# Kernel optimization log

Measured on AMD Instinct MI355X. Metric: run time of the kernel, lower is better.

## Reference

```python
import jax, jax.numpy as jnp
import numpy as np

NEG_SLOPE = 0.2
EPS = 1e-16


def gat_conv(x, src, dst, W, a_src, a_dst, b, num_nodes):
    # Single-head PyG GATConv (heads=1, add_self_loops already applied via src/dst).
    h = x @ W                                   # [N, C]
    alpha_s = h @ a_src                         # [N]
    alpha_d = h @ a_dst                         # [N]
    e = jax.nn.leaky_relu(alpha_s[src] + alpha_d[dst], NEG_SLOPE)  # [E]
    # softmax over incoming edges per destination node
    m = jax.ops.segment_max(e, dst, num_segments=num_nodes)        # [N]
    ex = jnp.exp(e - m[dst])
    denom = jax.ops.segment_sum(ex, dst, num_segments=num_nodes)   # [N]
    alpha = ex / (denom[dst] + EPS)                                 # [E]
    out = jax.ops.segment_sum(h[src] * alpha[:, None], dst, num_segments=num_nodes)
    return out + b


def setup_inputs() -> dict:
    key = jax.random.key(0)
    ks = jax.random.split(key, 10)
    N, E, F_in, H, C = 100000, 1600000, 64, 64, 32
    x = jax.random.normal(ks[0], (N, F_in), dtype=jnp.float32)
    edge_index = jax.random.randint(ks[1], (2, E), 0, N, dtype=jnp.int64)
    s1 = 1.0 / np.sqrt(F_in)
    s2 = 1.0 / np.sqrt(H)
    return {
        "x": x,
        "edge_index": edge_index,
        "W1": jax.random.normal(ks[2], (F_in, H), dtype=jnp.float32) * s1,
        "a1_src": jax.random.normal(ks[3], (H,), dtype=jnp.float32) * s2,
        "a1_dst": jax.random.normal(ks[4], (H,), dtype=jnp.float32) * s2,
        "b1": jnp.zeros((H,), dtype=jnp.float32),
        "W2": jax.random.normal(ks[5], (H, C), dtype=jnp.float32) * s2,
        "a2_src": jax.random.normal(ks[6], (C,), dtype=jnp.float32) / np.sqrt(C),
        "a2_dst": jax.random.normal(ks[7], (C,), dtype=jnp.float32) / np.sqrt(C),
        "b2": jnp.zeros((C,), dtype=jnp.float32),
    }


def reference(x, edge_index, W1, a1_src, a1_dst, b1, W2, a2_src, a2_dst, b2):
    N = x.shape[0]
    loops = jnp.arange(N, dtype=edge_index.dtype)
    src = jnp.concatenate([edge_index[0], loops])  # add self-loops (GATConv default)
    dst = jnp.concatenate([edge_index[1], loops])
    # dropout layers are no-ops in eval mode
    h = jax.nn.relu(gat_conv(x, src, dst, W1, a1_src, a1_dst, b1, N))
    out = gat_conv(h, src, dst, W2, a2_src, a2_dst, b2, N)
    return jax.nn.log_softmax(out, axis=-1)
```

## Files before the change

kernel.cpp:

```cpp
#include <hip/hip_runtime.h>

typedef unsigned int uint;
typedef unsigned short ushort;
typedef short short8 __attribute__((ext_vector_type(8)));
typedef float floatx4 __attribute__((ext_vector_type(4)));

#define LEAKY(e) ((e) > 0.f ? (e) : 0.2f * (e))
#define BCAP 6144
#define EPT 32
#define TILE (256 * EPT)

__device__ __forceinline__ ushort f2bf(float f) {
    uint u = __float_as_uint(f);
    return (ushort)((u + 0x7fffu + ((u >> 16) & 1u)) >> 16);
}
__device__ __forceinline__ uint pack2bf(float lo, float hi) {
    return (uint)f2bf(lo) | ((uint)f2bf(hi) << 16);
}
__device__ __forceinline__ float bflo(uint u) { return __uint_as_float(u << 16); }
__device__ __forceinline__ float bfhi(uint u) { return __uint_as_float(u & 0xffff0000u); }

__device__ __forceinline__ void binK_body(
    int bid, const int* __restrict__ srcA, const int* __restrict__ dstA,
    int* __restrict__ bcur, int* __restrict__ binned, int E, int Etot, int nbuck)
{
    __shared__ int hist[512];
    __shared__ int basep[512];
    int t = threadIdx.x;
    long long start = (long long)bid * TILE;

    hist[t] = 0; hist[t + 256] = 0;
    __syncthreads();

    short bs[EPT];
    int vals[EPT];
#pragma unroll
    for (int j = 0; j < EPT; ++j) {
        long long i = start + (long long)j * 256 + t;
        if (i < Etot) {
            int s, d;
            if (i < E) { s = srcA[i]; d = dstA[i]; } else { s = d = (int)(i - E); }
            int b = d >> 8;
            bs[j] = (short)b;
            vals[j] = (s << 8) | (d & 255);
            atomicAdd(&hist[b], 1);
        } else bs[j] = -1;
    }
    __syncthreads();

    for (int b = t; b < nbuck; b += 256) {
        int hc = hist[b];
        basep[b] = hc ? atomicAdd(bcur + b * 16, hc) : 0;
    }
    __syncthreads();
    hist[t] = 0; hist[t + 256] = 0;
    __syncthreads();

#pragma unroll
    for (int j = 0; j < EPT; ++j) {
        int b = bs[j];
        if (b >= 0) {
            int pos = basep[b] + atomicAdd(&hist[b], 1);
            if (pos < BCAP) binned[(size_t)b * BCAP + pos] = vals[j];
        }
    }
}

__device__ __forceinline__ void gemm1_body(
    int bid, const float* __restrict__ x, const float* __restrict__ W,
    const float* __restrict__ a_src, const float* __restrict__ a_dst,
    ushort* __restrict__ hb, float* __restrict__ as, float* __restrict__ ad, int N)
{
    int tid = threadIdx.x;
    int wave = tid >> 6, lane = tid & 63;
    int q = lane >> 4, c0 = lane & 15;
    int rowbase = bid * 64 + wave * 16;
    int arow = rowbase + c0;
    bool aok = arow < N;

    short8 afrag[2];
#pragma unroll
    for (int kb = 0; kb < 2; ++kb) {
        float xa[8];
        if (aok) {
            const float4 u0 = *(const float4*)(x + (size_t)arow * 64 + kb * 32 + q * 8);
            const float4 u1 = *(const float4*)(x + (size_t)arow * 64 + kb * 32 + q * 8 + 4);
            xa[0] = u0.x; xa[1] = u0.y; xa[2] = u0.z; xa[3] = u0.w;
            xa[4] = u1.x; xa[5] = u1.y; xa[6] = u1.z; xa[7] = u1.w;
        } else {
#pragma unroll
            for (int j = 0; j < 8; ++j) xa[j] = 0.f;
        }
#pragma unroll
        for (int j = 0; j < 8; ++j) afrag[kb][j] = (short)f2bf(xa[j]);
    }

    short8 bfrag[4][2];
#pragma unroll
    for (int t = 0; t < 4; ++t)
#pragma unroll
        for (int kb = 0; kb < 2; ++kb)
#pragma unroll
            for (int j = 0; j < 8; ++j)
                bfrag[t][kb][j] = (short)f2bf(W[(size_t)(kb * 32 + q * 8 + j) * 64 + t * 16 + c0]);

    floatx4 acc[4];
#pragma unroll
    for (int t = 0; t < 4; ++t) acc[t] = (floatx4){0.f, 0.f, 0.f, 0.f};
#pragma unroll
    for (int t = 0; t < 4; ++t)
#pragma unroll
        for (int kb = 0; kb < 2; ++kb)
            acc[t] = __builtin_amdgcn_mfma_f32_16x16x32_bf16(afrag[kb], bfrag[t][kb], acc[t], 0, 0, 0);

    float a_s[4], a_d[4];
#pragma unroll
    for (int t = 0; t < 4; ++t) { a_s[t] = a_src[t * 16 + c0]; a_d[t] = a_dst[t * 16 + c0]; }
    float vs[4], vd[4];
#pragma unroll
    for (int r = 0; r < 4; ++r) {
        vs[r] = 0.f; vd[r] = 0.f;
#pragma unroll
        for (int t = 0; t < 4; ++t) { vs[r] += acc[t][r] * a_s[t]; vd[r] += acc[t][r] * a_d[t]; }
    }
#pragma unroll
    for (int o = 1; o < 16; o <<= 1)
#pragma unroll
        for (int r = 0; r < 4; ++r) {
            vs[r] += __shfl_xor(vs[r], o, 16);
            vd[r] += __shfl_xor(vd[r], o, 16);
        }
    int drow = rowbase + q * 4;
    if (c0 == 0) {
#pragma unroll
        for (int r = 0; r < 4; ++r)
            if (drow + r < N) { as[drow + r] = vs[r]; ad[drow + r] = vd[r]; }
    }
#pragma unroll
    for (int r = 0; r < 4; ++r) {
        if (drow + r < N) {
#pragma unroll
            for (int t = 0; t < 4; ++t)
                hb[(size_t)(drow + r) * 64 + t * 16 + c0] = f2bf(acc[t][r]);
        }
    }
}

__global__ __launch_bounds__(256) void fusedK(
    const int* __restrict__ srcA, const int* __restrict__ dstA,
    int* __restrict__ bcur, int* __restrict__ binned, int E, int Etot, int nbuck, int tb,
    const float* __restrict__ x, const float* __restrict__ W,
    const float* __restrict__ a_src, const float* __restrict__ a_dst,
    ushort* __restrict__ hb, float* __restrict__ as, float* __restrict__ ad, int N)
{
    int b = (int)blockIdx.x;
    if (b < tb) binK_body(b, srcA, dstA, bcur, binned, E, Etot, nbuck);
    else gemm1_body(b - tb, x, W, a_src, a_dst, hb, as, ad, N);
}

__global__ __launch_bounds__(256) void gemm2_mfma(
    const ushort* __restrict__ aggb, const float* __restrict__ b1,
    const float* __restrict__ W,
    const float* __restrict__ a_src, const float* __restrict__ a_dst,
    ushort* __restrict__ hb, float* __restrict__ as, float* __restrict__ ad, int N)
{
    int tid = threadIdx.x;
    int wave = tid >> 6, lane = tid & 63;
    int q = lane >> 4, c0 = lane & 15;
    int rowbase = blockIdx.x * 64 + wave * 16;
    int arow = rowbase + c0;
    bool aok = arow < N;

    short8 afrag[2];
#pragma unroll
    for (int kb = 0; kb < 2; ++kb) {
        float xa[8];
        const float4 b0 = *(const float4*)(b1 + kb * 32 + q * 8);
        const float4 b4 = *(const float4*)(b1 + kb * 32 + q * 8 + 4);
        if (aok) {
            const uint4 u = *(const uint4*)(aggb + (size_t)arow * 64 + kb * 32 + q * 8);
            xa[0] = bflo(u.x) + b0.x; xa[1] = bfhi(u.x) + b0.y;
            xa[2] = bflo(u.y) + b0.z; xa[3] = bfhi(u.y) + b0.w;
            xa[4] = bflo(u.z) + b4.x; xa[5] = bfhi(u.z) + b4.y;
            xa[6] = bflo(u.w) + b4.z; xa[7] = bfhi(u.w) + b4.w;
#pragma unroll
            for (int j = 0; j < 8; ++j) xa[j] = xa[j] > 0.f ? xa[j] : 0.f;
        } else {
#pragma unroll
            for (int j = 0; j < 8; ++j) xa[j] = 0.f;
        }
#pragma unroll
        for (int j = 0; j < 8; ++j) afrag[kb][j] = (short)f2bf(xa[j]);
    }

    short8 bfrag[2][2];
#pragma unroll
    for (int t = 0; t < 2; ++t)
#pragma unroll
        for (int kb = 0; kb < 2; ++kb)
#pragma unroll
            for (int j = 0; j < 8; ++j)
                bfrag[t][kb][j] = (short)f2bf(W[(size_t)(kb * 32 + q * 8 + j) * 32 + t * 16 + c0]);

    floatx4 acc[2];
#pragma unroll
    for (int t = 0; t < 2; ++t) acc[t] = (floatx4){0.f, 0.f, 0.f, 0.f};
#pragma unroll
    for (int t = 0; t < 2; ++t)
#pragma unroll
        for (int kb = 0; kb < 2; ++kb)
            acc[t] = __builtin_amdgcn_mfma_f32_16x16x32_bf16(afrag[kb], bfrag[t][kb], acc[t], 0, 0, 0);

    float a_s[2], a_d[2];
#pragma unroll
    for (int t = 0; t < 2; ++t) { a_s[t] = a_src[t * 16 + c0]; a_d[t] = a_dst[t * 16 + c0]; }
    float vs[4], vd[4];
#pragma unroll
    for (int r = 0; r < 4; ++r) {
        vs[r] = 0.f; vd[r] = 0.f;
#pragma unroll
        for (int t = 0; t < 2; ++t) { vs[r] += acc[t][r] * a_s[t]; vd[r] += acc[t][r] * a_d[t]; }
    }
#pragma unroll
    for (int o = 1; o < 16; o <<= 1)
#pragma unroll
        for (int r = 0; r < 4; ++r) {
            vs[r] += __shfl_xor(vs[r], o, 16);
            vd[r] += __shfl_xor(vd[r], o, 16);
        }
    int drow = rowbase + q * 4;
    if (c0 == 0) {
#pragma unroll
        for (int r = 0; r < 4; ++r)
            if (drow + r < N) { as[drow + r] = vs[r]; ad[drow + r] = vd[r]; }
    }
#pragma unroll
    for (int r = 0; r < 4; ++r) {
        if (drow + r < N) {
#pragma unroll
            for (int t = 0; t < 2; ++t)
                hb[(size_t)(drow + r) * 32 + t * 16 + c0] = f2bf(acc[t][r]);
        }
    }
}

__global__ __launch_bounds__(256) void bucketK(
    const int* __restrict__ bcur, const int* __restrict__ binned,
    int* __restrict__ off, int* __restrict__ csr, int N, int nbuck)
{
    __shared__ int hist[256];
    __shared__ int sh[256];
    __shared__ int cur[256];
    int b = blockIdx.x;
    int t = threadIdx.x;
    int cnt = min(bcur[b * 16], BCAP);
    const int* bin = binned + (size_t)b * BCAP;

    int partial = 0;
    for (int i = t; i < b; i += 256) partial += min(bcur[i * 16], BCAP);
    sh[t] = partial;
    __syncthreads();
#pragma unroll
    for (int o = 128; o > 0; o >>= 1) {
        if (t < o) sh[t] += sh[t + o];
        __syncthreads();
    }
    int base = sh[0];
    __syncthreads();

    hist[t] = 0;
    __syncthreads();
    for (int i = t; i < cnt; i += 256) atomicAdd(&hist[bin[i] & 255], 1);
    __syncthreads();
    int v = hist[t];
    sh[t] = v;
    __syncthreads();
#pragma unroll
    for (int o = 1; o < 256; o <<= 1) {
        int u = (t >= o) ? sh[t - o] : 0;
        __syncthreads();
        sh[t] += u;
        __syncthreads();
    }
    int excl = sh[t] - v;
    int d = b * 256 + t;
    if (d < N) off[d] = base + excl;
    if (b == nbuck - 1 && t == 0) off[N] = base + cnt;
    cur[t] = base + excl;
    __syncthreads();
    for (int i = t; i < cnt; i += 256) {
        int e = bin[i];
        int p = atomicAdd(&cur[e & 255], 1);
        csr[p] = e >> 8;
    }
}

__global__ __launch_bounds__(256) void node_agg1(
    const int* __restrict__ csr_src, const int* __restrict__ off,
    const float* __restrict__ as, const float* __restrict__ ad,
    const ushort* __restrict__ hb, ushort* __restrict__ aggb, int N)
{
    int tid = threadIdx.x;
    int lid = tid & 7;
    int n = blockIdx.x * 32 + (tid >> 3);
    if (n >= N) return;
    int p0 = off[n], p1 = off[n + 1];
    float adn = ad[n];

    float den = 0.f;
    float acc[8];
#pragma unroll
    for (int k = 0; k < 8; ++k) acc[k] = 0.f;

    int base = p0;
    for (; base + 8 <= p1; base += 8) {
        int s_l = csr_src[base + lid];
        float a_l = as[s_l];
        uint4 v[8];
#pragma unroll
        for (int j = 0; j < 8; ++j) {
            int s_j = __shfl(s_l, j, 8);
            v[j] = *(const uint4*)(hb + (size_t)s_j * 64 + lid * 8);
        }
        float w_l = __expf(LEAKY(a_l + adn));
        den += w_l;
#pragma unroll
        for (int j = 0; j < 8; ++j) {
            float w = __shfl(w_l, j, 8);
            acc[0] += w * bflo(v[j].x); acc[1] += w * bfhi(v[j].x);
            acc[2] += w * bflo(v[j].y); acc[3] += w * bfhi(v[j].y);
            acc[4] += w * bflo(v[j].z); acc[5] += w * bfhi(v[j].z);
            acc[6] += w * bflo(v[j].w); acc[7] += w * bfhi(v[j].w);
        }
    }
    int r = p1 - base;
    if (r) {
        int s_l = 0; float w_l = 0.f;
        if (lid < r) { s_l = csr_src[base + lid]; w_l = __expf(LEAKY(as[s_l] + adn)); }
        den += w_l;
#pragma unroll
        for (int j = 0; j < 8; ++j) {
            if (j < r) {
                int s_j = __shfl(s_l, j, 8);
                float w = __shfl(w_l, j, 8);
                const uint4 v = *(const uint4*)(hb + (size_t)s_j * 64 + lid * 8);
                acc[0] += w * bflo(v.x); acc[1] += w * bfhi(v.x);
                acc[2] += w * bflo(v.y); acc[3] += w * bfhi(v.y);
                acc[4] += w * bflo(v.z); acc[5] += w * bfhi(v.z);
                acc[6] += w * bflo(v.w); acc[7] += w * bfhi(v.w);
            }
        }
    }
#pragma unroll
    for (int o = 4; o > 0; o >>= 1) den += __shfl_xor(den, o, 8);
    float inv = 1.f / den;
    uint4 o4;
    o4.x = pack2bf(acc[0] * inv, acc[1] * inv);
    o4.y = pack2bf(acc[2] * inv, acc[3] * inv);
    o4.z = pack2bf(acc[4] * inv, acc[5] * inv);
    o4.w = pack2bf(acc[6] * inv, acc[7] * inv);
    *(uint4*)(aggb + (size_t)n * 64 + lid * 8) = o4;
}

__global__ __launch_bounds__(256) void node_agg2(
    const int* __restrict__ csr_src, const int* __restrict__ off,
    const float* __restrict__ as, const float* __restrict__ ad,
    const ushort* __restrict__ hb, const float* __restrict__ b2,
    float* __restrict__ out, int N)
{
    int tid = threadIdx.x;
    int lid = tid & 3;
    int n = blockIdx.x * 64 + (tid >> 2);
    if (n >= N) return;
    int p0 = off[n], p1 = off[n + 1];
    float adn = ad[n];

    float den = 0.f;
    float acc[8];
#pragma unroll
    for (int k = 0; k < 8; ++k) acc[k] = 0.f;

    int base = p0;
    for (; base + 4 <= p1; base += 4) {
        int s_l = csr_src[base + lid];
        float a_l = as[s_l];
        uint4 v[4];
#pragma unroll
        for (int j = 0; j < 4; ++j) {
            int s_j = __shfl(s_l, j, 4);
            v[j] = *(const uint4*)(hb + (size_t)s_j * 32 + lid * 8);
        }
        float w_l = __expf(LEAKY(a_l + adn));
        den += w_l;
#pragma unroll
        for (int j = 0; j < 4; ++j) {
            float w = __shfl(w_l, j, 4);
            acc[0] += w * bflo(v[j].x); acc[1] += w * bfhi(v[j].x);
            acc[2] += w * bflo(v[j].y); acc[3] += w * bfhi(v[j].y);
            acc[4] += w * bflo(v[j].z); acc[5] += w * bfhi(v[j].z);
            acc[6] += w * bflo(v[j].w); acc[7] += w * bfhi(v[j].w);
        }
    }
    int r = p1 - base;
    if (r) {
        int s_l = 0; float w_l = 0.f;
        if (lid < r) { s_l = csr_src[base + lid]; w_l = __expf(LEAKY(as[s_l] + adn)); }
        den += w_l;
#pragma unroll
        for (int j = 0; j < 4; ++j) {
            if (j < r) {
                int s_j = __shfl(s_l, j, 4);
                float w = __shfl(w_l, j, 4);
                const uint4 v = *(const uint4*)(hb + (size_t)s_j * 32 + lid * 8);
                acc[0] += w * bflo(v.x); acc[1] += w * bfhi(v.x);
                acc[2] += w * bflo(v.y); acc[3] += w * bfhi(v.y);
                acc[4] += w * bflo(v.z); acc[5] += w * bfhi(v.z);
                acc[6] += w * bflo(v.w); acc[7] += w * bfhi(v.w);
            }
        }
    }
#pragma unroll
    for (int o = 2; o > 0; o >>= 1) den += __shfl_xor(den, o, 4);
    float inv = 1.f / den;
#pragma unroll
    for (int k = 0; k < 8; ++k) acc[k] = acc[k] * inv + b2[lid * 8 + k];

    float mx = acc[0];
#pragma unroll
    for (int k = 1; k < 8; ++k) mx = fmaxf(mx, acc[k]);
#pragma unroll
    for (int o = 2; o > 0; o >>= 1) mx = fmaxf(mx, __shfl_xor(mx, o, 4));
    float se = 0.f;
#pragma unroll
    for (int k = 0; k < 8; ++k) se += __expf(acc[k] - mx);
#pragma unroll
    for (int o = 2; o > 0; o >>= 1) se += __shfl_xor(se, o, 4);
    float lse = mx + __logf(se);
    float4 o0 = make_float4(acc[0] - lse, acc[1] - lse, acc[2] - lse, acc[3] - lse);
    float4 o1 = make_float4(acc[4] - lse, acc[5] - lse, acc[6] - lse, acc[7] - lse);
    float* op = out + (size_t)n * 32 + lid * 8;
    *(float4*)op = o0;
    *(float4*)(op + 4) = o1;
}

extern "C" void kernel_launch(void* const* d_in, const int* in_sizes, int n_in,
                              void* d_out, int out_size, void* d_ws, size_t ws_size,
                              hipStream_t stream) {
    const float* x   = (const float*)d_in[0];
    const int*   ei  = (const int*)d_in[1];
    const float* W1  = (const float*)d_in[2];
    const float* a1s = (const float*)d_in[3];
    const float* a1d = (const float*)d_in[4];
    const float* b1  = (const float*)d_in[5];
    const float* W2  = (const float*)d_in[6];
    const float* a2s = (const float*)d_in[7];
    const float* a2d = (const float*)d_in[8];
    const float* b2  = (const float*)d_in[9];

    int N = in_sizes[0] / 64;
    int E = in_sizes[1] / 2;
    int Etot = E + N;
    int nbuck = (N + 255) >> 8;
    const int* srcA = ei;
    const int* dstA = ei + E;

    float* ws = (float*)d_ws;
    ushort* hb1  = (ushort*)ws;
    ushort* aggb = hb1 + (size_t)N * 64;
    ushort* hb2  = aggb + (size_t)N * 64;
    float* as1   = ws + (size_t)N * (32 + 32 + 16);
    float* ad1   = as1 + N;
    float* as2   = ad1 + N;
    float* ad2   = as2 + N;
    int* off     = (int*)(ad2 + N);
    int* bcur    = off + (N + 1);
    int* csr     = bcur + (size_t)nbuck * 16;
    int* binned  = csr + Etot;

    hipMemsetAsync(bcur, 0, sizeof(int) * (size_t)nbuck * 16, stream);

    int tb = (int)(((long long)Etot + TILE - 1) / TILE);
    int g1 = (N + 63) / 64;

    fusedK<<<tb + g1, 256, 0, stream>>>(srcA, dstA, bcur, binned, E, Etot, nbuck, tb,
                                        x, W1, a1s, a1d, hb1, as1, ad1, N);
    bucketK<<<nbuck, 256, 0, stream>>>(bcur, binned, off, csr, N, nbuck);
    node_agg1<<<(N + 31) / 32, 256, 0, stream>>>(csr, off, as1, ad1, hb1, aggb, N);
    gemm2_mfma<<<g1, 256, 0, stream>>>(aggb, b1, W2, a2s, a2d, hb2, as2, ad2, N);
    node_agg2<<<(N + 63) / 64, 256, 0, stream>>>(csr, off, as2, ad2, hb2, b2,
                                                 (float*)d_out, N);
}
```

Baseline: 213.2 us.

## Fuse layer-1 aggregation with layer-2 GEMM into a single MFMA kernel

Merges node_agg1 and gemm2_mfma into one kernel. Each wave aggregates 16 destination nodes, with lanes laid out to match the MFMA A-fragment, so the aggregated features stay in registers and feed the layer-2 bf16 MFMA directly. This removes the write and re-read of the bf16 intermediate aggregation buffer and one kernel launch. The cost is a different gather pattern: 4 edges per iteration per node, a ballot-driven loop that runs to the highest degree among the wave's 16 nodes (divergence), and more registers per thread.

```diff
diff --git a/kernel.cpp b/kernel.cpp
--- a/kernel.cpp
+++ b/kernel.cpp
@@ -13,9 +13,6 @@
 __device__ __forceinline__ ushort f2bf(float f) {
     uint u = __float_as_uint(f);
     return (ushort)((u + 0x7fffu + ((u >> 16) & 1u)) >> 16);
-}
-__device__ __forceinline__ uint pack2bf(float lo, float hi) {
-    return (uint)f2bf(lo) | ((uint)f2bf(hi) << 16);
 }
 __device__ __forceinline__ float bflo(uint u) { return __uint_as_float(u << 16); }
 __device__ __forceinline__ float bfhi(uint u) { return __uint_as_float(u & 0xffff0000u); }
@@ -158,92 +155,6 @@
     else gemm1_body(b - tb, x, W, a_src, a_dst, hb, as, ad, N);
 }
 
-__global__ __launch_bounds__(256) void gemm2_mfma(
-    const ushort* __restrict__ aggb, const float* __restrict__ b1,
-    const float* __restrict__ W,
-    const float* __restrict__ a_src, const float* __restrict__ a_dst,
-    ushort* __restrict__ hb, float* __restrict__ as, float* __restrict__ ad, int N)
-{
-    int tid = threadIdx.x;
-    int wave = tid >> 6, lane = tid & 63;
-    int q = lane >> 4, c0 = lane & 15;
-    int rowbase = blockIdx.x * 64 + wave * 16;
-    int arow = rowbase + c0;
-    bool aok = arow < N;
-
-    short8 afrag[2];
-#pragma unroll
-    for (int kb = 0; kb < 2; ++kb) {
-        float xa[8];
-        const float4 b0 = *(const float4*)(b1 + kb * 32 + q * 8);
-        const float4 b4 = *(const float4*)(b1 + kb * 32 + q * 8 + 4);
-        if (aok) {
-            const uint4 u = *(const uint4*)(aggb + (size_t)arow * 64 + kb * 32 + q * 8);
-            xa[0] = bflo(u.x) + b0.x; xa[1] = bfhi(u.x) + b0.y;
-            xa[2] = bflo(u.y) + b0.z; xa[3] = bfhi(u.y) + b0.w;
-            xa[4] = bflo(u.z) + b4.x; xa[5] = bfhi(u.z) + b4.y;
-            xa[6] = bflo(u.w) + b4.z; xa[7] = bfhi(u.w) + b4.w;
-#pragma unroll
-            for (int j = 0; j < 8; ++j) xa[j] = xa[j] > 0.f ? xa[j] : 0.f;
-        } else {
-#pragma unroll
-            for (int j = 0; j < 8; ++j) xa[j] = 0.f;
-        }
-#pragma unroll
-        for (int j = 0; j < 8; ++j) afrag[kb][j] = (short)f2bf(xa[j]);
-    }
-
-    short8 bfrag[2][2];
-#pragma unroll
-    for (int t = 0; t < 2; ++t)
-#pragma unroll
-        for (int kb = 0; kb < 2; ++kb)
-#pragma unroll
-            for (int j = 0; j < 8; ++j)
-                bfrag[t][kb][j] = (short)f2bf(W[(size_t)(kb * 32 + q * 8 + j) * 32 + t * 16 + c0]);
-
-    floatx4 acc[2];
-#pragma unroll
-    for (int t = 0; t < 2; ++t) acc[t] = (floatx4){0.f, 0.f, 0.f, 0.f};
-#pragma unroll
-    for (int t = 0; t < 2; ++t)
-#pragma unroll
-        for (int kb = 0; kb < 2; ++kb)
-            acc[t] = __builtin_amdgcn_mfma_f32_16x16x32_bf16(afrag[kb], bfrag[t][kb], acc[t], 0, 0, 0);
-
-    float a_s[2], a_d[2];
-#pragma unroll
-    for (int t = 0; t < 2; ++t) { a_s[t] = a_src[t * 16 + c0]; a_d[t] = a_dst[t * 16 + c0]; }
-    float vs[4], vd[4];
-#pragma unroll
-    for (int r = 0; r < 4; ++r) {
-        vs[r] = 0.f; vd[r] = 0.f;
-#pragma unroll
-        for (int t = 0; t < 2; ++t) { vs[r] += acc[t][r] * a_s[t]; vd[r] += acc[t][r] * a_d[t]; }
-    }
-#pragma unroll
-    for (int o = 1; o < 16; o <<= 1)
-#pragma unroll
-        for (int r = 0; r < 4; ++r) {
-            vs[r] += __shfl_xor(vs[r], o, 16);
-            vd[r] += __shfl_xor(vd[r], o, 16);
-        }
-    int drow = rowbase + q * 4;
-    if (c0 == 0) {
-#pragma unroll
-        for (int r = 0; r < 4; ++r)
-            if (drow + r < N) { as[drow + r] = vs[r]; ad[drow + r] = vd[r]; }
-    }
-#pragma unroll
-    for (int r = 0; r < 4; ++r) {
-        if (drow + r < N) {
-#pragma unroll
-            for (int t = 0; t < 2; ++t)
-                hb[(size_t)(drow + r) * 32 + t * 16 + c0] = f2bf(acc[t][r]);
-        }
-    }
-}
-
 __global__ __launch_bounds__(256) void bucketK(
     const int* __restrict__ bcur, const int* __restrict__ binned,
     int* __restrict__ off, int* __restrict__ csr, int N, int nbuck)
@@ -295,71 +206,119 @@
     }
 }
 
-__global__ __launch_bounds__(256) void node_agg1(
-    const int* __restrict__ csr_src, const int* __restrict__ off,
+__global__ __launch_bounds__(256) void agg1gemm2K(
+    const int* __restrict__ csr, const int* __restrict__ off,
     const float* __restrict__ as, const float* __restrict__ ad,
-    const ushort* __restrict__ hb, ushort* __restrict__ aggb, int N)
+    const ushort* __restrict__ hb1, const float* __restrict__ b1,
+    const float* __restrict__ W,
+    const float* __restrict__ a_src, const float* __restrict__ a_dst,
+    ushort* __restrict__ hb2, float* __restrict__ as2, float* __restrict__ ad2, int N)
 {
     int tid = threadIdx.x;
-    int lid = tid & 7;
-    int n = blockIdx.x * 32 + (tid >> 3);
-    if (n >= N) return;
-    int p0 = off[n], p1 = off[n + 1];
-    float adn = ad[n];
+    int wave = tid >> 6, lane = tid & 63;
+    int q = lane >> 4, m = lane & 15;
+    int rowbase = blockIdx.x * 64 + wave * 16;
+    int n = rowbase + m;
+    int nc = (n < N) ? n : N - 1;
+    int p0 = off[nc];
+    int deg = (n < N) ? (off[nc + 1] - p0) : 0;
+    float adn = (n < N) ? ad[n] : 0.f;
 
     float den = 0.f;
-    float acc[8];
-#pragma unroll
-    for (int k = 0; k < 8; ++k) acc[k] = 0.f;
-
-    int base = p0;
-    for (; base + 8 <= p1; base += 8) {
-        int s_l = csr_src[base + lid];
-        float a_l = as[s_l];
-        uint4 v[8];
-#pragma unroll
-        for (int j = 0; j < 8; ++j) {
-            int s_j = __shfl(s_l, j, 8);
-            v[j] = *(const uint4*)(hb + (size_t)s_j * 64 + lid * 8);
-        }
-        float w_l = __expf(LEAKY(a_l + adn));
+    float acc0[8], acc1[8];
+#pragma unroll
+    for (int k = 0; k < 8; ++k) { acc0[k] = 0.f; acc1[k] = 0.f; }
+
+    int base = 0;
+    while (__ballot(base < deg)) {
+        bool valid = (base + q) < deg;
+        int s_l = valid ? csr[p0 + base + q] : 0;
+        float w_l = valid ? __expf(LEAKY(as[s_l] + adn)) : 0.f;
         den += w_l;
-#pragma unroll
-        for (int j = 0; j < 8; ++j) {
-            float w = __shfl(w_l, j, 8);
-            acc[0] += w * bflo(v[j].x); acc[1] += w * bfhi(v[j].x);
-            acc[2] += w * bflo(v[j].y); acc[3] += w * bfhi(v[j].y);
-            acc[4] += w * bflo(v[j].z); acc[5] += w * bfhi(v[j].z);
-            acc[6] += w * bflo(v[j].w); acc[7] += w * bfhi(v[j].w);
-        }
-    }
-    int r = p1 - base;
-    if (r) {
-        int s_l = 0; float w_l = 0.f;
-        if (lid < r) { s_l = csr_src[base + lid]; w_l = __expf(LEAKY(as[s_l] + adn)); }
-        den += w_l;
-#pragma unroll
-        for (int j = 0; j < 8; ++j) {
-            if (j < r) {
-                int s_j = __shfl(s_l, j, 8);
-                float w = __shfl(w_l, j, 8);
-                const uint4 v = *(const uint4*)(hb + (size_t)s_j * 64 + lid * 8);
-                acc[0] += w * bflo(v.x); acc[1] += w * bfhi(v.x);
-                acc[2] += w * bflo(v.y); acc[3] += w * bfhi(v.y);
-                acc[4] += w * bflo(v.z); acc[5] += w * bfhi(v.z);
-                acc[6] += w * bflo(v.w); acc[7] += w * bfhi(v.w);
-            }
-        }
-    }
-#pragma unroll
-    for (int o = 4; o > 0; o >>= 1) den += __shfl_xor(den, o, 8);
+        int sj[4];
+        uint4 va[4], vb[4];
+#pragma unroll
+        for (int j = 0; j < 4; ++j) {
+            sj[j] = __shfl(s_l, m | (j << 4), 64);
+            va[j] = *(const uint4*)(hb1 + (size_t)sj[j] * 64 + q * 8);
+            vb[j] = *(const uint4*)(hb1 + (size_t)sj[j] * 64 + 32 + q * 8);
+        }
+#pragma unroll
+        for (int j = 0; j < 4; ++j) {
+            float w = __shfl(w_l, m | (j << 4), 64);
+            acc0[0] += w * bflo(va[j].x); acc0[1] += w * bfhi(va[j].x);
+            acc0[2] += w * bflo(va[j].y); acc0[3] += w * bfhi(va[j].y);
+            acc0[4] += w * bflo(va[j].z); acc0[5] += w * bfhi(va[j].z);
+            acc0[6] += w * bflo(va[j].w); acc0[7] += w * bfhi(va[j].w);
+            acc1[0] += w * bflo(vb[j].x); acc1[1] += w * bfhi(vb[j].x);
+            acc1[2] += w * bflo(vb[j].y); acc1[3] += w * bfhi(vb[j].y);
+            acc1[4] += w * bflo(vb[j].z); acc1[5] += w * bfhi(vb[j].z);
+            acc1[6] += w * bflo(vb[j].w); acc1[7] += w * bfhi(vb[j].w);
+        }
+        base += 4;
+    }
+    den += __shfl_xor(den, 16, 64);
+    den += __shfl_xor(den, 32, 64);
     float inv = 1.f / den;
-    uint4 o4;
-    o4.x = pack2bf(acc[0] * inv, acc[1] * inv);
-    o4.y = pack2bf(acc[2] * inv, acc[3] * inv);
-    o4.z = pack2bf(acc[4] * inv, acc[5] * inv);
-    o4.w = pack2bf(acc[6] * inv, acc[7] * inv);
-    *(uint4*)(aggb + (size_t)n * 64 + lid * 8) = o4;
+
+    short8 afrag[2];
+#pragma unroll
+    for (int j = 0; j < 8; ++j) {
+        float x0 = acc0[j] * inv + b1[q * 8 + j];
+        float x1 = acc1[j] * inv + b1[32 + q * 8 + j];
+        afrag[0][j] = (short)f2bf(x0 > 0.f ? x0 : 0.f);
+        afrag[1][j] = (short)f2bf(x1 > 0.f ? x1 : 0.f);
+    }
+
+    short8 bfrag[2][2];
+#pragma unroll
+    for (int t = 0; t < 2; ++t)
+#pragma unroll
+        for (int kb = 0; kb < 2; ++kb)
+#pragma unroll
+            for (int j = 0; j < 8; ++j)
+                bfrag[t][kb][j] = (short)f2bf(W[(size_t)(kb * 32 + q * 8 + j) * 32 + t * 16 + m]);
+
+    floatx4 acc[2];
+#pragma unroll
+    for (int t = 0; t < 2; ++t) acc[t] = (floatx4){0.f, 0.f, 0.f, 0.f};
+#pragma unroll
+    for (int t = 0; t < 2; ++t)
+#pragma unroll
+        for (int kb = 0; kb < 2; ++kb)
+            acc[t] = __builtin_amdgcn_mfma_f32_16x16x32_bf16(afrag[kb], bfrag[t][kb], acc[t], 0, 0, 0);
+
+    float a_s[2], a_d[2];
+#pragma unroll
+    for (int t = 0; t < 2; ++t) { a_s[t] = a_src[t * 16 + m]; a_d[t] = a_dst[t * 16 + m]; }
+    float vs[4], vd[4];
+#pragma unroll
+    for (int r = 0; r < 4; ++r) {
+        vs[r] = 0.f; vd[r] = 0.f;
+#pragma unroll
+        for (int t = 0; t < 2; ++t) { vs[r] += acc[t][r] * a_s[t]; vd[r] += acc[t][r] * a_d[t]; }
+    }
+#pragma unroll
+    for (int o = 1; o < 16; o <<= 1)
+#pragma unroll
+        for (int r = 0; r < 4; ++r) {
+            vs[r] += __shfl_xor(vs[r], o, 16);
+            vd[r] += __shfl_xor(vd[r], o, 16);
+        }
+    int drow = rowbase + q * 4;
+    if (m == 0) {
+#pragma unroll
+        for (int r = 0; r < 4; ++r)
+            if (drow + r < N) { as2[drow + r] = vs[r]; ad2[drow + r] = vd[r]; }
+    }
+#pragma unroll
+    for (int r = 0; r < 4; ++r) {
+        if (drow + r < N) {
+#pragma unroll
+            for (int t = 0; t < 2; ++t)
+                hb2[(size_t)(drow + r) * 32 + t * 16 + m] = f2bf(acc[t][r]);
+        }
+    }
 }
 
 __global__ __launch_bounds__(256) void node_agg2(
@@ -465,17 +424,16 @@
     const int* dstA = ei + E;
 
     float* ws = (float*)d_ws;
-    ushort* hb1  = (ushort*)ws;
-    ushort* aggb = hb1 + (size_t)N * 64;
-    ushort* hb2  = aggb + (size_t)N * 64;
-    float* as1   = ws + (size_t)N * (32 + 32 + 16);
-    float* ad1   = as1 + N;
-    float* as2   = ad1 + N;
-    float* ad2   = as2 + N;
-    int* off     = (int*)(ad2 + N);
-    int* bcur    = off + (N + 1);
-    int* csr     = bcur + (size_t)nbuck * 16;
-    int* binned  = csr + Etot;
+    ushort* hb1 = (ushort*)ws;
+    ushort* hb2 = hb1 + (size_t)N * 64;
+    float* as1  = ws + (size_t)N * 48;
+    float* ad1  = as1 + N;
+    float* as2  = ad1 + N;
+    float* ad2  = as2 + N;
+    int* off    = (int*)(ad2 + N);
+    int* bcur   = off + (N + 1);
+    int* csr    = bcur + (size_t)nbuck * 16;
+    int* binned = csr + Etot;
 
     hipMemsetAsync(bcur, 0, sizeof(int) * (size_t)nbuck * 16, stream);
 
@@ -485,8 +443,8 @@
     fusedK<<<tb + g1, 256, 0, stream>>>(srcA, dstA, bcur, binned, E, Etot, nbuck, tb,
                                         x, W1, a1s, a1d, hb1, as1, ad1, N);
     bucketK<<<nbuck, 256, 0, stream>>>(bcur, binned, off, csr, N, nbuck);
-    node_agg1<<<(N + 31) / 32, 256, 0, stream>>>(csr, off, as1, ad1, hb1, aggb, N);
-    gemm2_mfma<<<g1, 256, 0, stream>>>(aggb, b1, W2, a2s, a2d, hb2, as2, ad2, N);
+    agg1gemm2K<<<g1, 256, 0, stream>>>(csr, off, as1, ad1, hb1, b1, W2, a2s, a2d,
+                                       hb2, as2, ad2, N);
     node_agg2<<<(N + 63) / 64, 256, 0, stream>>>(csr, off, as2, ad2, hb2, b2,
                                                  (float*)d_out, N);
 }
```

Result: slower. 219.0 us (+2.7%).

## Fuse layer-1 aggregation with layer-2 MFMA GEMM via shared memory

Applied to the files above, without the earlier changes.

Merges node_agg1 and gemm2_mfma into one kernel. The per-node aggregated layer-1 features are staged in LDS in fp32 and then consumed by two waves running the 64x32 MFMA projection, bias, ReLU and attention-logit reductions. This removes one launch and the bf16 round trip of the N x 64 intermediate through global memory. In exchange, two of the four waves sit idle during the GEMM phase and the block needs a barrier and about 8.7 KB of LDS.

```diff
diff --git a/kernel.cpp b/kernel.cpp
--- a/kernel.cpp
+++ b/kernel.cpp
@@ -13,9 +13,6 @@
 __device__ __forceinline__ ushort f2bf(float f) {
     uint u = __float_as_uint(f);
     return (ushort)((u + 0x7fffu + ((u >> 16) & 1u)) >> 16);
-}
-__device__ __forceinline__ uint pack2bf(float lo, float hi) {
-    return (uint)f2bf(lo) | ((uint)f2bf(hi) << 16);
 }
 __device__ __forceinline__ float bflo(uint u) { return __uint_as_float(u << 16); }
 __device__ __forceinline__ float bfhi(uint u) { return __uint_as_float(u & 0xffff0000u); }
@@ -158,92 +155,6 @@
     else gemm1_body(b - tb, x, W, a_src, a_dst, hb, as, ad, N);
 }
 
-__global__ __launch_bounds__(256) void gemm2_mfma(
-    const ushort* __restrict__ aggb, const float* __restrict__ b1,
-    const float* __restrict__ W,
-    const float* __restrict__ a_src, const float* __restrict__ a_dst,
-    ushort* __restrict__ hb, float* __restrict__ as, float* __restrict__ ad, int N)
-{
-    int tid = threadIdx.x;
-    int wave = tid >> 6, lane = tid & 63;
-    int q = lane >> 4, c0 = lane & 15;
-    int rowbase = blockIdx.x * 64 + wave * 16;
-    int arow = rowbase + c0;
-    bool aok = arow < N;
-
-    short8 afrag[2];
-#pragma unroll
-    for (int kb = 0; kb < 2; ++kb) {
-        float xa[8];
-        const float4 b0 = *(const float4*)(b1 + kb * 32 + q * 8);
-        const float4 b4 = *(const float4*)(b1 + kb * 32 + q * 8 + 4);
-        if (aok) {
-            const uint4 u = *(const uint4*)(aggb + (size_t)arow * 64 + kb * 32 + q * 8);
-            xa[0] = bflo(u.x) + b0.x; xa[1] = bfhi(u.x) + b0.y;
-            xa[2] = bflo(u.y) + b0.z; xa[3] = bfhi(u.y) + b0.w;
-            xa[4] = bflo(u.z) + b4.x; xa[5] = bfhi(u.z) + b4.y;
-            xa[6] = bflo(u.w) + b4.z; xa[7] = bfhi(u.w) + b4.w;
-#pragma unroll
-            for (int j = 0; j < 8; ++j) xa[j] = xa[j] > 0.f ? xa[j] : 0.f;
-        } else {
-#pragma unroll
-            for (int j = 0; j < 8; ++j) xa[j] = 0.f;
-        }
-#pragma unroll
-        for (int j = 0; j < 8; ++j) afrag[kb][j] = (short)f2bf(xa[j]);
-    }
-
-    short8 bfrag[2][2];
-#pragma unroll
-    for (int t = 0; t < 2; ++t)
-#pragma unroll
-        for (int kb = 0; kb < 2; ++kb)
-#pragma unroll
-            for (int j = 0; j < 8; ++j)
-                bfrag[t][kb][j] = (short)f2bf(W[(size_t)(kb * 32 + q * 8 + j) * 32 + t * 16 + c0]);
-
-    floatx4 acc[2];
-#pragma unroll
-    for (int t = 0; t < 2; ++t) acc[t] = (floatx4){0.f, 0.f, 0.f, 0.f};
-#pragma unroll
-    for (int t = 0; t < 2; ++t)
-#pragma unroll
-        for (int kb = 0; kb < 2; ++kb)
-            acc[t] = __builtin_amdgcn_mfma_f32_16x16x32_bf16(afrag[kb], bfrag[t][kb], acc[t], 0, 0, 0);
-
-    float a_s[2], a_d[2];
-#pragma unroll
-    for (int t = 0; t < 2; ++t) { a_s[t] = a_src[t * 16 + c0]; a_d[t] = a_dst[t * 16 + c0]; }
-    float vs[4], vd[4];
-#pragma unroll
-    for (int r = 0; r < 4; ++r) {
-        vs[r] = 0.f; vd[r] = 0.f;
-#pragma unroll
-        for (int t = 0; t < 2; ++t) { vs[r] += acc[t][r] * a_s[t]; vd[r] += acc[t][r] * a_d[t]; }
-    }
-#pragma unroll
-    for (int o = 1; o < 16; o <<= 1)
-#pragma unroll
-        for (int r = 0; r < 4; ++r) {
-            vs[r] += __shfl_xor(vs[r], o, 16);
-            vd[r] += __shfl_xor(vd[r], o, 16);
-        }
-    int drow = rowbase + q * 4;
-    if (c0 == 0) {
-#pragma unroll
-        for (int r = 0; r < 4; ++r)
-            if (drow + r < N) { as[drow + r] = vs[r]; ad[drow + r] = vd[r]; }
-    }
-#pragma unroll
-    for (int r = 0; r < 4; ++r) {
-        if (drow + r < N) {
-#pragma unroll
-            for (int t = 0; t < 2; ++t)
-                hb[(size_t)(drow + r) * 32 + t * 16 + c0] = f2bf(acc[t][r]);
-        }
-    }
-}
-
 __global__ __launch_bounds__(256) void bucketK(
     const int* __restrict__ bcur, const int* __restrict__ binned,
     int* __restrict__ off, int* __restrict__ csr, int N, int nbuck)
@@ -295,71 +206,142 @@
     }
 }
 
-__global__ __launch_bounds__(256) void node_agg1(
+__global__ __launch_bounds__(256) void agg1gemm2K(
     const int* __restrict__ csr_src, const int* __restrict__ off,
     const float* __restrict__ as, const float* __restrict__ ad,
-    const ushort* __restrict__ hb, ushort* __restrict__ aggb, int N)
-{
+    const ushort* __restrict__ hb1, const float* __restrict__ b1,
+    const float* __restrict__ W,
+    const float* __restrict__ a_src, const float* __restrict__ a_dst,
+    ushort* __restrict__ hb2, float* __restrict__ as2, float* __restrict__ ad2, int N)
+{
+    __shared__ float aggL[32 * 68];
     int tid = threadIdx.x;
     int lid = tid & 7;
-    int n = blockIdx.x * 32 + (tid >> 3);
-    if (n >= N) return;
-    int p0 = off[n], p1 = off[n + 1];
-    float adn = ad[n];
+    int nl = tid >> 3;
+    int n = blockIdx.x * 32 + nl;
 
     float den = 0.f;
     float acc[8];
 #pragma unroll
     for (int k = 0; k < 8; ++k) acc[k] = 0.f;
 
-    int base = p0;
-    for (; base + 8 <= p1; base += 8) {
-        int s_l = csr_src[base + lid];
-        float a_l = as[s_l];
-        uint4 v[8];
+    if (n < N) {
+        int p0 = off[n], p1 = off[n + 1];
+        float adn = ad[n];
+        int base = p0;
+        for (; base + 8 <= p1; base += 8) {
+            int s_l = csr_src[base + lid];
+            float a_l = as[s_l];
+            uint4 v[8];
+#pragma unroll
+            for (int j = 0; j < 8; ++j) {
+                int s_j = __shfl(s_l, j, 8);
+                v[j] = *(const uint4*)(hb1 + (size_t)s_j * 64 + lid * 8);
+            }
+            float w_l = __expf(LEAKY(a_l + adn));
+            den += w_l;
+#pragma unroll
+            for (int j = 0; j < 8; ++j) {
+                float w = __shfl(w_l, j, 8);
+                acc[0] += w * bflo(v[j].x); acc[1] += w * bfhi(v[j].x);
+                acc[2] += w * bflo(v[j].y); acc[3] += w * bfhi(v[j].y);
+                acc[4] += w * bflo(v[j].z); acc[5] += w * bfhi(v[j].z);
+                acc[6] += w * bflo(v[j].w); acc[7] += w * bfhi(v[j].w);
+            }
+        }
+        int r = p1 - base;
+        if (r) {
+            int s_l = 0; float w_l = 0.f;
+            if (lid < r) { s_l = csr_src[base + lid]; w_l = __expf(LEAKY(as[s_l] + adn)); }
+            den += w_l;
+#pragma unroll
+            for (int j = 0; j < 8; ++j) {
+                if (j < r) {
+                    int s_j = __shfl(s_l, j, 8);
+                    float w = __shfl(w_l, j, 8);
+                    const uint4 v = *(const uint4*)(hb1 + (size_t)s_j * 64 + lid * 8);
+                    acc[0] += w * bflo(v.x); acc[1] += w * bfhi(v.x);
+                    acc[2] += w * bflo(v.y); acc[3] += w * bfhi(v.y);
+                    acc[4] += w * bflo(v.z); acc[5] += w * bfhi(v.z);
+                    acc[6] += w * bflo(v.w); acc[7] += w * bfhi(v.w);
+                }
+            }
+        }
+#pragma unroll
+        for (int o = 4; o > 0; o >>= 1) den += __shfl_xor(den, o, 8);
+    } else den = 1.f;
+
+    float inv = 1.f / den;
+    float4 o0 = make_float4(acc[0] * inv, acc[1] * inv, acc[2] * inv, acc[3] * inv);
+    float4 o1 = make_float4(acc[4] * inv, acc[5] * inv, acc[6] * inv, acc[7] * inv);
+    *(float4*)&aggL[nl * 68 + lid * 8] = o0;
+    *(float4*)&aggL[nl * 68 + lid * 8 + 4] = o1;
+    __syncthreads();
+
+    int wave = tid >> 6, lane = tid & 63;
+    if (wave >= 2) return;
+    int q = lane >> 4, m = lane & 15;
+    int rowbase = blockIdx.x * 32 + wave * 16;
+
+    short8 afrag[2];
+#pragma unroll
+    for (int kb = 0; kb < 2; ++kb) {
 #pragma unroll
         for (int j = 0; j < 8; ++j) {
-            int s_j = __shfl(s_l, j, 8);
-            v[j] = *(const uint4*)(hb + (size_t)s_j * 64 + lid * 8);
-        }
-        float w_l = __expf(LEAKY(a_l + adn));
-        den += w_l;
-#pragma unroll
-        for (int j = 0; j < 8; ++j) {
-            float w = __shfl(w_l, j, 8);
-            acc[0] += w * bflo(v[j].x); acc[1] += w * bfhi(v[j].x);
-            acc[2] += w * bflo(v[j].y); acc[3] += w * bfhi(v[j].y);
-            acc[4] += w * bflo(v[j].z); acc[5] += w * bfhi(v[j].z);
-            acc[6] += w * bflo(v[j].w); acc[7] += w * bfhi(v[j].w);
-        }
-    }
-    int r = p1 - base;
-    if (r) {
-        int s_l = 0; float w_l = 0.f;
-        if (lid < r) { s_l = csr_src[base + lid]; w_l = __expf(LEAKY(as[s_l] + adn)); }
-        den += w_l;
-#pragma unroll
-        for (int j = 0; j < 8; ++j) {
-            if (j < r) {
-                int s_j = __shfl(s_l, j, 8);
-                float w = __shfl(w_l, j, 8);
-                const uint4 v = *(const uint4*)(hb + (size_t)s_j * 64 + lid * 8);
-                acc[0] += w * bflo(v.x); acc[1] += w * bfhi(v.x);
-                acc[2] += w * bflo(v.y); acc[3] += w * bfhi(v.y);
-                acc[4] += w * bflo(v.z); acc[5] += w * bfhi(v.z);
-                acc[6] += w * bflo(v.w); acc[7] += w * bfhi(v.w);
-            }
-        }
-    }
-#pragma unroll
-    for (int o = 4; o > 0; o >>= 1) den += __shfl_xor(den, o, 8);
-    float inv = 1.f / den;
-    uint4 o4;
-    o4.x = pack2bf(acc[0] * inv, acc[1] * inv);
-    o4.y = pack2bf(acc[2] * inv, acc[3] * inv);
-    o4.z = pack2bf(acc[4] * inv, acc[5] * inv);
-    o4.w = pack2bf(acc[6] * inv, acc[7] * inv);
-    *(uint4*)(aggb + (size_t)n * 64 + lid * 8) = o4;
+            float xv = aggL[(wave * 16 + m) * 68 + kb * 32 + q * 8 + j] + b1[kb * 32 + q * 8 + j];
+            afrag[kb][j] = (short)f2bf(xv > 0.f ? xv : 0.f);
+        }
+    }
+
+    short8 bfrag[2][2];
+#pragma unroll
+    for (int t = 0; t < 2; ++t)
+#pragma unroll
+        for (int kb = 0; kb < 2; ++kb)
+#pragma unroll
+            for (int j = 0; j < 8; ++j)
+                bfrag[t][kb][j] = (short)f2bf(W[(size_t)(kb * 32 + q * 8 + j) * 32 + t * 16 + m]);
+
+    floatx4 cacc[2];
+#pragma unroll
+    for (int t = 0; t < 2; ++t) cacc[t] = (floatx4){0.f, 0.f, 0.f, 0.f};
+#pragma unroll
+    for (int t = 0; t < 2; ++t)
+#pragma unroll
+        for (int kb = 0; kb < 2; ++kb)
+            cacc[t] = __builtin_amdgcn_mfma_f32_16x16x32_bf16(afrag[kb], bfrag[t][kb], cacc[t], 0, 0, 0);
+
+    float a_s[2], a_d[2];
+#pragma unroll
+    for (int t = 0; t < 2; ++t) { a_s[t] = a_src[t * 16 + m]; a_d[t] = a_dst[t * 16 + m]; }
+    float vs[4], vd[4];
+#pragma unroll
+    for (int r = 0; r < 4; ++r) {
+        vs[r] = 0.f; vd[r] = 0.f;
+#pragma unroll
+        for (int t = 0; t < 2; ++t) { vs[r] += cacc[t][r] * a_s[t]; vd[r] += cacc[t][r] * a_d[t]; }
+    }
+#pragma unroll
+    for (int o = 1; o < 16; o <<= 1)
+#pragma unroll
+        for (int r = 0; r < 4; ++r) {
+            vs[r] += __shfl_xor(vs[r], o, 16);
+            vd[r] += __shfl_xor(vd[r], o, 16);
+        }
+    int drow = rowbase + q * 4;
+    if (m == 0) {
+#pragma unroll
+        for (int r = 0; r < 4; ++r)
+            if (drow + r < N) { as2[drow + r] = vs[r]; ad2[drow + r] = vd[r]; }
+    }
+#pragma unroll
+    for (int r = 0; r < 4; ++r) {
+        if (drow + r < N) {
+#pragma unroll
+            for (int t = 0; t < 2; ++t)
+                hb2[(size_t)(drow + r) * 32 + t * 16 + m] = f2bf(cacc[t][r]);
+        }
+    }
 }
 
 __global__ __launch_bounds__(256) void node_agg2(
@@ -465,17 +447,16 @@
     const int* dstA = ei + E;
 
     float* ws = (float*)d_ws;
-    ushort* hb1  = (ushort*)ws;
-    ushort* aggb = hb1 + (size_t)N * 64;
-    ushort* hb2  = aggb + (size_t)N * 64;
-    float* as1   = ws + (size_t)N * (32 + 32 + 16);
-    float* ad1   = as1 + N;
-    float* as2   = ad1 + N;
-    float* ad2   = as2 + N;
-    int* off     = (int*)(ad2 + N);
-    int* bcur    = off + (N + 1);
-    int* csr     = bcur + (size_t)nbuck * 16;
-    int* binned  = csr + Etot;
+    ushort* hb1 = (ushort*)ws;
+    ushort* hb2 = hb1 + (size_t)N * 64;
+    float* as1  = ws + (size_t)N * 48;
+    float* ad1  = as1 + N;
+    float* as2  = ad1 + N;
+    float* ad2  = as2 + N;
+    int* off    = (int*)(ad2 + N);
+    int* bcur   = off + (N + 1);
+    int* csr    = bcur + (size_t)nbuck * 16;
+    int* binned = csr + Etot;
 
     hipMemsetAsync(bcur, 0, sizeof(int) * (size_t)nbuck * 16, stream);
 
@@ -485,8 +466,8 @@
     fusedK<<<tb + g1, 256, 0, stream>>>(srcA, dstA, bcur, binned, E, Etot, nbuck, tb,
                                         x, W1, a1s, a1d, hb1, as1, ad1, N);
     bucketK<<<nbuck, 256, 0, stream>>>(bcur, binned, off, csr, N, nbuck);
-    node_agg1<<<(N + 31) / 32, 256, 0, stream>>>(csr, off, as1, ad1, hb1, aggb, N);
-    gemm2_mfma<<<g1, 256, 0, stream>>>(aggb, b1, W2, a2s, a2d, hb2, as2, ad2, N);
+    agg1gemm2K<<<(N + 31) / 32, 256, 0, stream>>>(csr, off, as1, ad1, hb1, b1, W2,
+                                                  a2s, a2d, hb2, as2, ad2, N);
     node_agg2<<<(N + 63) / 64, 256, 0, stream>>>(csr, off, as2, ad2, hb2, b2,
                                                  (float*)d_out, N);
 }
```

Result: no change. 209.1 us (-1.9%).
